# Kernel tuning notes

Hardware: AMD Instinct MI355X
Metric: run time of the kernel (lower is better)

The kernel has to match this reference:

```python
import jax, jax.numpy as jnp
import numpy as np

EMBED = 512
HEADS = 8
HEAD_DIM = EMBED // HEADS
WINDOW = 256
HALF = WINDOW // 2
B, S = 2, 2048


def setup_inputs() -> dict:
    key = jax.random.key(0)
    kv, kk, kq, kw = jax.random.split(key, 4)
    return {
        "values": jax.random.normal(kv, (B, 1, S, EMBED), dtype=jnp.float32),
        "keys": jax.random.normal(kk, (B, 1, S, EMBED), dtype=jnp.float32),
        "query": jax.random.normal(kq, (B, 1, S, EMBED), dtype=jnp.float32),
        "mask": jnp.ones((B, 1, 1, S), dtype=jnp.int32),
        "fc_w": jax.random.normal(kw, (EMBED, EMBED), dtype=jnp.float32) * (1.0 / np.sqrt(EMBED)),
        "fc_b": jnp.zeros((EMBED,), dtype=jnp.float32),
    }


def reference(values, keys, query, mask, fc_w, fc_b):
    b = query.shape[0]
    s = values.shape[2]
    v = values.reshape(b, s, HEADS, HEAD_DIM)
    k = keys.reshape(b, s, HEADS, HEAD_DIM)
    q = query.reshape(b, s, HEADS, HEAD_DIM)
    scale = jnp.float32(EMBED ** 0.5)

    # global token: query 0 attends to all keys
    gq = q[:, 0:1]  # (b,1,h,d)
    ge = jnp.einsum('bqhd,bkhd->bhqk', gq, k)
    ga = jax.nn.softmax(ge / scale, axis=3)
    gout = jnp.einsum('bhqk,bkhd->bqhd', ga, v)  # (b,1,h,d)

    # sliding-window queries (positions 1..s-1, band centered at local index i)
    wq = q[:, 1:]  # (b, s-1, h, d)
    qw = s - 1
    e = jnp.einsum('bqhd,bkhd->bhqk', wq, k)  # (b,h,qw,s)
    i = jnp.arange(qw)[:, None]
    j = jnp.arange(s)[None, :]
    band = (j >= i - HALF) & (j <= i + HALF)  # (qw, s)
    # faithful to original: out-of-band energies are ZERO (not -inf)
    e = jnp.where(band[None, None], e, jnp.float32(0.0))
    e = jnp.where(mask == 0, jnp.float32(-1e20), e)
    a = jax.nn.softmax(e / scale, axis=3)
    lout = jnp.einsum('bhqk,bkhd->bqhd', a, v)  # (b,qw,h,d)

    out = jnp.concatenate([gout, lout], axis=1).reshape(b, s, HEADS * HEAD_DIM)
    return out @ fc_w.T + fc_b
```

## Files before the change

### kernel.cpp

```cpp
#include <hip/hip_runtime.h>
#include <math.h>

#define EMBED 512
#define HEADS 8
#define HDIM 64
#define SLEN 2048
#define BATCH 2
#define HALFW 128
#define NCHUNK 32
#define INV_SCALE 0.044194173824159216f

typedef short bf16x8 __attribute__((ext_vector_type(8)));
typedef short s16x4  __attribute__((ext_vector_type(4)));
typedef float f32x4  __attribute__((ext_vector_type(4)));

#define MFMA16(a, b, c) __builtin_amdgcn_mfma_f32_16x16x32_bf16(a, b, c, 0, 0, 0)

__device__ __forceinline__ short f2bf(float x) {
    union { float f; unsigned u; } v; v.f = x;
    unsigned r = v.u + 0x7FFFu + ((v.u >> 16) & 1u);
    return (short)(r >> 16);
}

__device__ __forceinline__ int lidx(int row, int seg) {
    return (((seg << 6) + (row ^ seg)) << 3);
}

__device__ __forceinline__ void gll16(const short* g, short* l) {
    __builtin_amdgcn_global_load_lds(
        (const __attribute__((address_space(1))) unsigned int*)g,
        (__attribute__((address_space(3))) unsigned int*)l, 16, 0, 0);
}

__device__ __forceinline__ void stage_chunk(const short* s0, const short* s1,
                                            short* d0, short* d1, int t) {
    int off = t * 8;
    int wb  = (t >> 6) * 512;
    gll16(s0 + off,        d0 + wb);
    gll16(s0 + 2048 + off, d0 + 2048 + wb);
    gll16(s1 + off,        d1 + wb);
    gll16(s1 + 2048 + off, d1 + 2048 + wb);
}

__global__ __launch_bounds__(256) void prepass(
    const float* __restrict__ q, const float* __restrict__ k,
    const float* __restrict__ v, const int* __restrict__ mask,
    const float* __restrict__ fcw,
    short* __restrict__ Kbf, short* __restrict__ Vbf, short* __restrict__ Wbf,
    float* __restrict__ gnum_part, float* __restrict__ gden_part,
    float* __restrict__ vsum_part, float* __restrict__ nval_part) {
    int d = blockIdx.x;
    int x = d & 7, i = d >> 3;
    int hb8 = x * 2 + (i >= 36);
    int c   = (i >= 36) ? (i - 36) : i;
    int h = hb8 & 7, b = hb8 >> 3;
    int t = threadIdx.x, w = t >> 6, l = t & 63;

    if (c >= NCHUNK) {
        int nb = b * 4 + (c - NCHUNK);
        size_t base = (size_t)(nb * 8 + h) * 4096;
        #pragma unroll
        for (int p = 0; p < 4; ++p) {
            int idx = p * 256 + t, row = idx >> 4, kg = idx & 15;
            float4 f = *(const float4*)(fcw + (size_t)(nb * 64 + row) * EMBED + h * 64 + kg * 4);
            s16x4 o;
            o[0] = f2bf(f.x); o[1] = f2bf(f.y); o[2] = f2bf(f.z); o[3] = f2bf(f.w);
            *(s16x4*)&Wbf[base + lidx(row, kg >> 1) + (kg & 1) * 4] = o;
        }
        return;
    }

    int j0 = c * 64;
    __shared__ float q0s[HDIM];
    __shared__ float wls[64];
    __shared__ int   m_s[64];
    __shared__ float vbuf[64][68];
    __shared__ float red[4][HDIM];
    __shared__ float redv[4][HDIM];

    if (t < 64) {
        q0s[t] = q[(size_t)b * SLEN * EMBED + h * HDIM + t];
        m_s[t] = mask[b * SLEN + j0 + t];
    }
    __syncthreads();

    size_t fragbase = ((size_t)(b * HEADS + h) * NCHUNK + c) * 4096;

    #pragma unroll
    for (int p = 0; p < 4; ++p) {
        int idx = p * 256 + t, row = idx >> 4, kg = idx & 15;
        float4 f = *(const float4*)(k + ((size_t)b * SLEN + j0 + row) * EMBED + h * HDIM + kg * 4);
        float dot = q0s[kg*4+0]*f.x + q0s[kg*4+1]*f.y + q0s[kg*4+2]*f.z + q0s[kg*4+3]*f.w;
        dot += __shfl_xor(dot, 1, 64);
        dot += __shfl_xor(dot, 2, 64);
        dot += __shfl_xor(dot, 4, 64);
        dot += __shfl_xor(dot, 8, 64);
        if ((t & 15) == 0) wls[row] = __expf(dot * INV_SCALE);
        if (!m_s[row]) f = make_float4(0.f, 0.f, 0.f, 0.f);
        s16x4 o;
        o[0] = f2bf(f.x); o[1] = f2bf(f.y); o[2] = f2bf(f.z); o[3] = f2bf(f.w);
        *(s16x4*)&Kbf[fragbase + lidx(row, kg >> 1) + (kg & 1) * 4] = o;
    }

    #pragma unroll
    for (int p = 0; p < 4; ++p) {
        int idx = p * 256 + t, row = idx >> 4, kg = idx & 15;
        float4 f = *(const float4*)(v + ((size_t)b * SLEN + j0 + row) * EMBED + h * HDIM + kg * 4);
        *(float4*)&vbuf[row][kg * 4] = f;
    }
    __syncthreads();

    float num = 0.f, vs = 0.f;
    #pragma unroll
    for (int jj = 0; jj < 16; ++jj) {
        int jl = w * 16 + jj;
        float vv = vbuf[jl][l];
        num += wls[jl] * vv;
        if (m_s[jl]) vs += vv;
    }
    red[w][l] = num;
    redv[w][l] = vs;

    #pragma unroll
    for (int s = 0; s < 2; ++s) {
        int jseg = w * 2 + s;
        bf16x8 o;
        #pragma unroll
        for (int e = 0; e < 8; ++e) o[e] = f2bf(vbuf[jseg * 8 + e][l]);
        *(bf16x8*)&Vbf[fragbase + lidx(l, jseg)] = o;
    }
    __syncthreads();

    if (w == 0) {
        gnum_part[((size_t)(b * HEADS + h) * NCHUNK + c) * HDIM + l] =
            red[0][l] + red[1][l] + red[2][l] + red[3][l];
        vsum_part[((size_t)b * NCHUNK + c) * EMBED + h * HDIM + l] =
            redv[0][l] + redv[1][l] + redv[2][l] + redv[3][l];
    } else if (w == 1) {
        float s = wls[l];
        #pragma unroll
        for (int off = 32; off > 0; off >>= 1) s += __shfl_xor(s, off, 64);
        if (l == 0) gden_part[(size_t)(b * HEADS + h) * NCHUNK + c] = s;
    } else if (w == 2 && h == 0) {
        float cc = m_s[l] ? 1.f : 0.f;
        #pragma unroll
        for (int off = 32; off > 0; off >>= 1) cc += __shfl_xor(cc, off, 64);
        if (l == 0) nval_part[b * NCHUNK + c] = cc;
    }
}

__global__ __launch_bounds__(256) void windowed_attn_v8(
    const float* __restrict__ q, const float* __restrict__ k,
    const float* __restrict__ v, const int* __restrict__ mask,
    const short* __restrict__ Kbf, const short* __restrict__ Vbf,
    const float* __restrict__ gnum_part, const float* __restrict__ gden_part,
    const float* __restrict__ vsum_part, const float* __restrict__ nval_part,
    short* __restrict__ Abf) {
    int dsp = blockIdx.x;
    int wid = (dsp & 7) * 64 + (dsp >> 3);
    int tile = wid & 31, h = (wid >> 5) & 7, b = wid >> 8;
    int r0 = tile * 64;
    int t = threadIdx.x, w = t >> 6, l = t & 63;
    int lg = l >> 4, lr = l & 15;

    __shared__ __align__(16) short k_s[4][4096];
    __shared__ __align__(16) short v_s[4][4096];
    __shared__ __align__(16) short wT_s[4][16][72];
    __shared__ float rsum[64];
    __shared__ float vred[4][64];
    __shared__ float gred[4][64];
    __shared__ float nv_s, gd_s;

    size_t hb = (size_t)(b * HEADS + h) * NCHUNK;
    int bh = b * HEADS + h;

    int c0 = tile - 2; if (c0 < 0) c0 = 0;
    int c1 = tile + 2; if (c1 > NCHUNK - 1) c1 = NCHUNK - 1;

    stage_chunk(Kbf + (hb + c0) * 4096, Vbf + (hb + c0) * 4096,
                &k_s[0][0], &v_s[0][0], t);

    const float* qrow = q + ((size_t)b * SLEN + r0 + w * 16 + lr) * EMBED + h * HDIM;
    float4 a0 = *(const float4*)(qrow + lg * 8);
    float4 a1 = *(const float4*)(qrow + lg * 8 + 4);
    float4 a2 = *(const float4*)(qrow + 32 + lg * 8);
    float4 a3 = *(const float4*)(qrow + 32 + lg * 8 + 4);
    bf16x8 qb0, qb1;
    qb0[0] = f2bf(a0.x); qb0[1] = f2bf(a0.y); qb0[2] = f2bf(a0.z); qb0[3] = f2bf(a0.w);
    qb0[4] = f2bf(a1.x); qb0[5] = f2bf(a1.y); qb0[6] = f2bf(a1.z); qb0[7] = f2bf(a1.w);
    qb1[0] = f2bf(a2.x); qb1[1] = f2bf(a2.y); qb1[2] = f2bf(a2.z); qb1[3] = f2bf(a2.w);
    qb1[4] = f2bf(a3.x); qb1[5] = f2bf(a3.y); qb1[6] = f2bf(a3.z); qb1[7] = f2bf(a3.w);

    {
        float vp = 0.f;
        #pragma unroll
        for (int cc = 0; cc < 8; ++cc)
            vp += vsum_part[((size_t)b * NCHUNK + w * 8 + cc) * EMBED + h * HDIM + l];
        vred[w][l] = vp;
        if (w == 0) {
            float nvv = (l < NCHUNK) ? nval_part[b * NCHUNK + l] : 0.f;
            #pragma unroll
            for (int off = 32; off > 0; off >>= 1) nvv += __shfl_xor(nvv, off, 64);
            if (l == 0) nv_s = nvv;
        }
        if (tile == 0) {
            float gp = 0.f;
            #pragma unroll
            for (int cc = 0; cc < 8; ++cc)
                gp += gnum_part[((size_t)bh * NCHUNK + w * 8 + cc) * HDIM + l];
            gred[w][l] = gp;
            if (w == 1) {
                float gdd = (l < NCHUNK) ? gden_part[(size_t)bh * NCHUNK + l] : 0.f;
                #pragma unroll
                for (int off = 32; off > 0; off >>= 1) gdd += __shfl_xor(gdd, off, 64);
                if (l == 0) gd_s = gdd;
            }
        }
    }

    stage_chunk(Kbf + (hb + c0 + 1) * 4096, Vbf + (hb + c0 + 1) * 4096,
                &k_s[1][0], &v_s[1][0], t);
    stage_chunk(Kbf + (hb + c0 + 2) * 4096, Vbf + (hb + c0 + 2) * 4096,
                &k_s[2][0], &v_s[2][0], t);

    int center = r0 + w * 16 + lr - 1;
    int lo = center - HALFW, hi = center + HALFW;

    f32x4 pv[4];
    #pragma unroll
    for (int dt = 0; dt < 4; ++dt) pv[dt] = (f32x4){0.f, 0.f, 0.f, 0.f};
    float dacc = 0.f;

    int bi = 0;
    for (int c = c0; c <= c1; ++c) {
        int rem = c1 - c;
        if (rem >= 2)      { asm volatile("s_waitcnt vmcnt(8)" ::: "memory"); }
        else if (rem == 1) { asm volatile("s_waitcnt vmcnt(4)" ::: "memory"); }
        else               { asm volatile("s_waitcnt vmcnt(0)" ::: "memory"); }
        __syncthreads();

        int jc = c * 64;
        #pragma unroll
        for (int jt = 0; jt < 4; ++jt) {
            bf16x8 ka0 = *(const bf16x8*)&k_s[bi][lidx(jt * 16 + lr, lg)];
            bf16x8 ka1 = *(const bf16x8*)&k_s[bi][lidx(jt * 16 + lr, 4 + lg)];
            f32x4 sT = (f32x4){0.f, 0.f, 0.f, 0.f};
            sT = MFMA16(ka0, qb0, sT);
            sT = MFMA16(ka1, qb1, sT);
            int jbase = jc + jt * 16 + lg * 4;
            s16x4 wq;
            #pragma unroll
            for (int r = 0; r < 4; ++r) {
                int j = jbase + r;
                float wgt = (j >= lo && j <= hi) ? (__expf(sT[r] * INV_SCALE) - 1.f) : 0.f;
                dacc += wgt;
                wq[r] = f2bf(wgt);
            }
            *(s16x4*)&wT_s[w][lr][jt * 16 + lg * 4] = wq;
        }

        bf16x8 wa0 = *(const bf16x8*)&wT_s[w][lr][lg * 8];
        bf16x8 wa1 = *(const bf16x8*)&wT_s[w][lr][32 + lg * 8];
        #pragma unroll
        for (int dt = 0; dt < 4; ++dt) {
            bf16x8 va0 = *(const bf16x8*)&v_s[bi][lidx(dt * 16 + lr, lg)];
            bf16x8 va1 = *(const bf16x8*)&v_s[bi][lidx(dt * 16 + lr, 4 + lg)];
            pv[dt] = MFMA16(wa0, va0, pv[dt]);
            pv[dt] = MFMA16(wa1, va1, pv[dt]);
        }

        if (c + 3 <= c1) {
            int bn = (bi + 3) & 3;
            stage_chunk(Kbf + (hb + c + 3) * 4096, Vbf + (hb + c + 3) * 4096,
                        &k_s[bn][0], &v_s[bn][0], t);
        }
        bi = (bi + 1) & 3;
    }

    float wfix = 0.f;
    int jx = r0 - 129;
    if (w == 0 && jx >= 0) {
        float qv = q[((size_t)b * SLEN + r0) * EMBED + h * HDIM + l];
        float kv = k[((size_t)b * SLEN + jx) * EMBED + h * HDIM + l];
        float dd = qv * kv;
        #pragma unroll
        for (int off = 32; off > 0; off >>= 1) dd += __shfl_xor(dd, off, 64);
        if (mask[b * SLEN + jx] != 0) wfix = __expf(dd * INV_SCALE) - 1.f;
        if (lg == 0) {
            #pragma unroll
            for (int dt = 0; dt < 4; ++dt)
                pv[dt][0] += wfix * v[((size_t)b * SLEN + jx) * EMBED + h * HDIM + dt * 16 + lr];
        }
    }

    dacc += __shfl_xor(dacc, 16, 64);
    dacc += __shfl_xor(dacc, 32, 64);
    if (lg == 0) rsum[w * 16 + lr] = dacc + ((w == 0 && lr == 0) ? wfix : 0.f);
    __syncthreads();

    float nv = nv_s;
    float invden[4];
    #pragma unroll
    for (int r = 0; r < 4; ++r)
        invden[r] = 1.f / (nv + rsum[w * 16 + lg * 4 + r]);

    short* Atile = Abf + ((size_t)(b * NCHUNK + tile) * 8 + h) * 4096;
    #pragma unroll
    for (int dt = 0; dt < 4; ++dt) {
        int d = dt * 16 + lr;
        float vs = vred[0][d] + vred[1][d] + vred[2][d] + vred[3][d];
        #pragma unroll
        for (int r = 0; r < 4; ++r) {
            int row_local = w * 16 + lg * 4 + r;
            float o;
            if (tile == 0 && row_local == 0)
                o = (gred[0][d] + gred[1][d] + gred[2][d] + gred[3][d]) / gd_s;
            else
                o = (pv[dt][r] + vs) * invden[r];
            Atile[lidx(row_local, d >> 3) + (d & 7)] = f2bf(o);
        }
    }
}

__global__ __launch_bounds__(256) void fc_gemm_v4(
    const short* __restrict__ Abf, const short* __restrict__ Wbf,
    const float* __restrict__ bias, float* __restrict__ C) {
    int bm = blockIdx.x;
    int nb = blockIdx.y;
    int t = threadIdx.x, w = t >> 6, l = t & 63;
    int lg = l >> 4, lr = l & 15;
    int wr = w >> 1, wc = w & 1;

    __shared__ __align__(16) short a_s[8][4096];
    __shared__ __align__(16) short w_s[2][4096];

    int off = t * 8;
    int wb  = (t >> 6) * 512;

    #pragma unroll
    for (int kt = 0; kt < 8; ++kt) {
        const short* as = Abf + (size_t)(bm * 8 + kt) * 4096;
        gll16(as + off,        &a_s[kt][wb]);
        gll16(as + 2048 + off, &a_s[kt][2048 + wb]);
    }
    {
        const short* ws0 = Wbf + (size_t)(nb * 8 + 0) * 4096;
        gll16(ws0 + off,        &w_s[0][wb]);
        gll16(ws0 + 2048 + off, &w_s[0][2048 + wb]);
        const short* ws1 = Wbf + (size_t)(nb * 8 + 1) * 4096;
        gll16(ws1 + off,        &w_s[1][wb]);
        gll16(ws1 + 2048 + off, &w_s[1][2048 + wb]);
    }

    f32x4 acc[2][2];
    #pragma unroll
    for (int mt = 0; mt < 2; ++mt)
        #pragma unroll
        for (int nt = 0; nt < 2; ++nt) acc[mt][nt] = (f32x4){0.f, 0.f, 0.f, 0.f};

    for (int kt = 0; kt < 8; ++kt) {
        if (kt < 7) { asm volatile("s_waitcnt vmcnt(2)" ::: "memory"); }
        else        { asm volatile("s_waitcnt vmcnt(0)" ::: "memory"); }
        __syncthreads();

        bf16x8 af[2][2], bf_[2][2];
        #pragma unroll
        for (int mt = 0; mt < 2; ++mt) {
            af[mt][0] = *(const bf16x8*)&a_s[kt][lidx(wr * 32 + mt * 16 + lr, lg)];
            af[mt][1] = *(const bf16x8*)&a_s[kt][lidx(wr * 32 + mt * 16 + lr, 4 + lg)];
        }
        int wbuf = kt & 1;
        #pragma unroll
        for (int nt = 0; nt < 2; ++nt) {
            bf_[nt][0] = *(const bf16x8*)&w_s[wbuf][lidx(wc * 32 + nt * 16 + lr, lg)];
            bf_[nt][1] = *(const bf16x8*)&w_s[wbuf][lidx(wc * 32 + nt * 16 + lr, 4 + lg)];
        }
        #pragma unroll
        for (int mt = 0; mt < 2; ++mt)
            #pragma unroll
            for (int nt = 0; nt < 2; ++nt) {
                acc[mt][nt] = MFMA16(af[mt][0], bf_[nt][0], acc[mt][nt]);
                acc[mt][nt] = MFMA16(af[mt][1], bf_[nt][1], acc[mt][nt]);
            }

        __syncthreads();
        if (kt + 2 <= 7) {
            const short* ws = Wbf + (size_t)(nb * 8 + kt + 2) * 4096;
            gll16(ws + off,        &w_s[wbuf][wb]);
            gll16(ws + 2048 + off, &w_s[wbuf][2048 + wb]);
        }
    }

    #pragma unroll
    for (int mt = 0; mt < 2; ++mt)
        #pragma unroll
        for (int nt = 0; nt < 2; ++nt) {
            int n = nb * 64 + wc * 32 + nt * 16 + lr;
            float bb = bias[n];
            #pragma unroll
            for (int reg = 0; reg < 4; ++reg) {
                int m = bm * 64 + wr * 32 + mt * 16 + lg * 4 + reg;
                C[(size_t)m * 512 + n] = acc[mt][nt][reg] + bb;
            }
        }
}

extern "C" void kernel_launch(void* const* d_in, const int* in_sizes, int n_in,
                              void* d_out, int out_size, void* d_ws, size_t ws_size,
                              hipStream_t stream) {
    const float* values = (const float*)d_in[0];
    const float* keys   = (const float*)d_in[1];
    const float* query  = (const float*)d_in[2];
    const int*   maskp  = (const int*)d_in[3];
    const float* fc_w   = (const float*)d_in[4];
    const float* fc_b   = (const float*)d_in[5];
    float* out = (float*)d_out;

    short* Abf = (short*)d_ws;
    short* Wbf = Abf + (size_t)BATCH * SLEN * EMBED;
    short* Kbf = Wbf + (size_t)EMBED * EMBED;
    short* Vbf = Kbf + (size_t)BATCH * HEADS * NCHUNK * 4096;
    float* vsum_part = (float*)(Vbf + (size_t)BATCH * HEADS * NCHUNK * 4096);
    float* gnum_part = vsum_part + (size_t)BATCH * NCHUNK * EMBED;
    float* gden_part = gnum_part + (size_t)BATCH * HEADS * NCHUNK * HDIM;
    float* nval_part = gden_part + (size_t)BATCH * HEADS * NCHUNK;

    prepass<<<dim3(576), 256, 0, stream>>>(
        query, keys, values, maskp, fc_w, Kbf, Vbf, Wbf,
        gnum_part, gden_part, vsum_part, nval_part);
    windowed_attn_v8<<<dim3(512), 256, 0, stream>>>(
        query, keys, values, maskp, Kbf, Vbf,
        gnum_part, gden_part, vsum_part, nval_part, Abf);
    fc_gemm_v4<<<dim3(64, 8), 256, 0, stream>>>(
        Abf, Wbf, fc_b, out);
}
```

Baseline: 31.73 us.

## Split prepass into 32-row half-chunks and issue W tiles before A in GEMM

The prepass now processes 32-key half-chunks per block instead of 64, doubling its grid to 1088 blocks. Partial sums for the global token and vsum double in count, and the attention kernel reduces over 64 partials. The W-conversion blocks are also remapped. In the FC GEMM, the first two W tiles are issued right after the first A tile, with adjusted vmcnt waits, so the first k-steps can start sooner. The cost is more blocks with less work each and more partial-sum traffic.

After: 30.91 us (median of 2 runs). 1.03x faster.

```diff
diff --git a/kernel.cpp b/kernel.cpp
--- a/kernel.cpp
+++ b/kernel.cpp
@@ -40,6 +40,13 @@
     gll16(s0 + 2048 + off, d0 + 2048 + wb);
     gll16(s1 + off,        d1 + wb);
     gll16(s1 + 2048 + off, d1 + 2048 + wb);
+}
+
+__device__ __forceinline__ void stage_tile(const short* s, short* d, int t) {
+    int off = t * 8;
+    int wb  = (t >> 6) * 512;
+    gll16(s + off,        d + wb);
+    gll16(s + 2048 + off, d + 2048 + wb);
 }
 
 __global__ __launch_bounds__(256) void prepass(
@@ -51,18 +58,19 @@
     float* __restrict__ vsum_part, float* __restrict__ nval_part) {
     int d = blockIdx.x;
     int x = d & 7, i = d >> 3;
-    int hb8 = x * 2 + (i >= 36);
-    int c   = (i >= 36) ? (i - 36) : i;
+    int hb8 = x * 2 + (i >= 68);
+    int ii  = (i >= 68) ? (i - 68) : i;
     int h = hb8 & 7, b = hb8 >> 3;
     int t = threadIdx.x, w = t >> 6, l = t & 63;
 
-    if (c >= NCHUNK) {
-        int nb = b * 4 + (c - NCHUNK);
-        size_t base = (size_t)(nb * 8 + h) * 4096;
+    if (ii >= 64) {
+        int widx = hb8 * 4 + (ii - 64);
+        int nb = widx >> 3, kt = widx & 7;
+        size_t base = (size_t)(nb * 8 + kt) * 4096;
         #pragma unroll
         for (int p = 0; p < 4; ++p) {
             int idx = p * 256 + t, row = idx >> 4, kg = idx & 15;
-            float4 f = *(const float4*)(fcw + (size_t)(nb * 64 + row) * EMBED + h * 64 + kg * 4);
+            float4 f = *(const float4*)(fcw + (size_t)(nb * 64 + row) * EMBED + kt * 64 + kg * 4);
             s16x4 o;
             o[0] = f2bf(f.x); o[1] = f2bf(f.y); o[2] = f2bf(f.z); o[3] = f2bf(f.w);
             *(s16x4*)&Wbf[base + lidx(row, kg >> 1) + (kg & 1) * 4] = o;
@@ -70,24 +78,26 @@
         return;
     }
 
-    int j0 = c * 64;
+    int ch  = ii;
+    int c   = ch >> 1;
+    int rof = (ch & 1) * 32;
+    int j0  = ch * 32;
+
     __shared__ float q0s[HDIM];
-    __shared__ float wls[64];
-    __shared__ int   m_s[64];
-    __shared__ float vbuf[64][68];
+    __shared__ float wls[32];
+    __shared__ int   m_s[32];
+    __shared__ float vbuf[32][68];
     __shared__ float red[4][HDIM];
     __shared__ float redv[4][HDIM];
 
-    if (t < 64) {
-        q0s[t] = q[(size_t)b * SLEN * EMBED + h * HDIM + t];
-        m_s[t] = mask[b * SLEN + j0 + t];
-    }
+    if (t < 64) q0s[t] = q[(size_t)b * SLEN * EMBED + h * HDIM + t];
+    else if (t < 96) m_s[t - 64] = mask[b * SLEN + j0 + (t - 64)];
     __syncthreads();
 
     size_t fragbase = ((size_t)(b * HEADS + h) * NCHUNK + c) * 4096;
 
     #pragma unroll
-    for (int p = 0; p < 4; ++p) {
+    for (int p = 0; p < 2; ++p) {
         int idx = p * 256 + t, row = idx >> 4, kg = idx & 15;
         float4 f = *(const float4*)(k + ((size_t)b * SLEN + j0 + row) * EMBED + h * HDIM + kg * 4);
         float dot = q0s[kg*4+0]*f.x + q0s[kg*4+1]*f.y + q0s[kg*4+2]*f.z + q0s[kg*4+3]*f.w;
@@ -99,11 +109,11 @@
         if (!m_s[row]) f = make_float4(0.f, 0.f, 0.f, 0.f);
         s16x4 o;
         o[0] = f2bf(f.x); o[1] = f2bf(f.y); o[2] = f2bf(f.z); o[3] = f2bf(f.w);
-        *(s16x4*)&Kbf[fragbase + lidx(row, kg >> 1) + (kg & 1) * 4] = o;
-    }
-
-    #pragma unroll
-    for (int p = 0; p < 4; ++p) {
+        *(s16x4*)&Kbf[fragbase + lidx(rof + row, kg >> 1) + (kg & 1) * 4] = o;
+    }
+
+    #pragma unroll
+    for (int p = 0; p < 2; ++p) {
         int idx = p * 256 + t, row = idx >> 4, kg = idx & 15;
         float4 f = *(const float4*)(v + ((size_t)b * SLEN + j0 + row) * EMBED + h * HDIM + kg * 4);
         *(float4*)&vbuf[row][kg * 4] = f;
@@ -112,8 +122,8 @@
 
     float num = 0.f, vs = 0.f;
     #pragma unroll
-    for (int jj = 0; jj < 16; ++jj) {
-        int jl = w * 16 + jj;
+    for (int jj = 0; jj < 8; ++jj) {
+        int jl = w * 8 + jj;
         float vv = vbuf[jl][l];
         num += wls[jl] * vv;
         if (m_s[jl]) vs += vv;
@@ -121,35 +131,34 @@
     red[w][l] = num;
     redv[w][l] = vs;
 
-    #pragma unroll
-    for (int s = 0; s < 2; ++s) {
-        int jseg = w * 2 + s;
+    {
+        int jseg = (ch & 1) * 4 + w;
         bf16x8 o;
         #pragma unroll
-        for (int e = 0; e < 8; ++e) o[e] = f2bf(vbuf[jseg * 8 + e][l]);
+        for (int e = 0; e < 8; ++e) o[e] = f2bf(vbuf[w * 8 + e][l]);
         *(bf16x8*)&Vbf[fragbase + lidx(l, jseg)] = o;
     }
     __syncthreads();
 
     if (w == 0) {
-        gnum_part[((size_t)(b * HEADS + h) * NCHUNK + c) * HDIM + l] =
+        gnum_part[((size_t)(b * HEADS + h) * 64 + ch) * HDIM + l] =
             red[0][l] + red[1][l] + red[2][l] + red[3][l];
-        vsum_part[((size_t)b * NCHUNK + c) * EMBED + h * HDIM + l] =
+        vsum_part[((size_t)b * 64 + ch) * EMBED + h * HDIM + l] =
             redv[0][l] + redv[1][l] + redv[2][l] + redv[3][l];
     } else if (w == 1) {
-        float s = wls[l];
+        float s = (l < 32) ? wls[l] : 0.f;
         #pragma unroll
         for (int off = 32; off > 0; off >>= 1) s += __shfl_xor(s, off, 64);
-        if (l == 0) gden_part[(size_t)(b * HEADS + h) * NCHUNK + c] = s;
+        if (l == 0) gden_part[(size_t)(b * HEADS + h) * 64 + ch] = s;
     } else if (w == 2 && h == 0) {
-        float cc = m_s[l] ? 1.f : 0.f;
+        float cc = (l < 32 && m_s[l]) ? 1.f : 0.f;
         #pragma unroll
         for (int off = 32; off > 0; off >>= 1) cc += __shfl_xor(cc, off, 64);
-        if (l == 0) nval_part[b * NCHUNK + c] = cc;
-    }
-}
-
-__global__ __launch_bounds__(256) void windowed_attn_v8(
+        if (l == 0) nval_part[b * 64 + ch] = cc;
+    }
+}
+
+__global__ __launch_bounds__(256) void windowed_attn_v9(
     const float* __restrict__ q, const float* __restrict__ k,
     const float* __restrict__ v, const int* __restrict__ mask,
     const short* __restrict__ Kbf, const short* __restrict__ Vbf,
@@ -194,11 +203,11 @@
     {
         float vp = 0.f;
         #pragma unroll
-        for (int cc = 0; cc < 8; ++cc)
-            vp += vsum_part[((size_t)b * NCHUNK + w * 8 + cc) * EMBED + h * HDIM + l];
+        for (int cc = 0; cc < 16; ++cc)
+            vp += vsum_part[((size_t)b * 64 + w * 16 + cc) * EMBED + h * HDIM + l];
         vred[w][l] = vp;
         if (w == 0) {
-            float nvv = (l < NCHUNK) ? nval_part[b * NCHUNK + l] : 0.f;
+            float nvv = nval_part[b * 64 + l];
             #pragma unroll
             for (int off = 32; off > 0; off >>= 1) nvv += __shfl_xor(nvv, off, 64);
             if (l == 0) nv_s = nvv;
@@ -206,11 +215,11 @@
         if (tile == 0) {
             float gp = 0.f;
             #pragma unroll
-            for (int cc = 0; cc < 8; ++cc)
-                gp += gnum_part[((size_t)bh * NCHUNK + w * 8 + cc) * HDIM + l];
+            for (int cc = 0; cc < 16; ++cc)
+                gp += gnum_part[((size_t)bh * 64 + w * 16 + cc) * HDIM + l];
             gred[w][l] = gp;
             if (w == 1) {
-                float gdd = (l < NCHUNK) ? gden_part[(size_t)bh * NCHUNK + l] : 0.f;
+                float gdd = gden_part[(size_t)bh * 64 + l];
                 #pragma unroll
                 for (int off = 32; off > 0; off >>= 1) gdd += __shfl_xor(gdd, off, 64);
                 if (l == 0) gd_s = gdd;
@@ -322,7 +331,7 @@
     }
 }
 
-__global__ __launch_bounds__(256) void fc_gemm_v4(
+__global__ __launch_bounds__(256) void fc_gemm_v5(
     const short* __restrict__ Abf, const short* __restrict__ Wbf,
     const float* __restrict__ bias, float* __restrict__ C) {
     int bm = blockIdx.x;
@@ -334,33 +343,24 @@
     __shared__ __align__(16) short a_s[8][4096];
     __shared__ __align__(16) short w_s[2][4096];
 
-    int off = t * 8;
-    int wb  = (t >> 6) * 512;
-
-    #pragma unroll
+    stage_tile(Abf + (size_t)(bm * 8 + 0) * 4096, &a_s[0][0], t);
+    stage_tile(Wbf + (size_t)(nb * 8 + 0) * 4096, &w_s[0][0], t);
+    stage_tile(Wbf + (size_t)(nb * 8 + 1) * 4096, &w_s[1][0], t);
+    #pragma unroll
+    for (int kt = 1; kt < 8; ++kt)
+        stage_tile(Abf + (size_t)(bm * 8 + kt) * 4096, &a_s[kt][0], t);
+
+    f32x4 acc[2][2];
+    #pragma unroll
+    for (int mt = 0; mt < 2; ++mt)
+        #pragma unroll
+        for (int nt = 0; nt < 2; ++nt) acc[mt][nt] = (f32x4){0.f, 0.f, 0.f, 0.f};
+
     for (int kt = 0; kt < 8; ++kt) {
-        const short* as = Abf + (size_t)(bm * 8 + kt) * 4096;
-        gll16(as + off,        &a_s[kt][wb]);
-        gll16(as + 2048 + off, &a_s[kt][2048 + wb]);
-    }
-    {
-        const short* ws0 = Wbf + (size_t)(nb * 8 + 0) * 4096;
-        gll16(ws0 + off,        &w_s[0][wb]);
-        gll16(ws0 + 2048 + off, &w_s[0][2048 + wb]);
-        const short* ws1 = Wbf + (size_t)(nb * 8 + 1) * 4096;
-        gll16(ws1 + off,        &w_s[1][wb]);
-        gll16(ws1 + 2048 + off, &w_s[1][2048 + wb]);
-    }
-
-    f32x4 acc[2][2];
-    #pragma unroll
-    for (int mt = 0; mt < 2; ++mt)
-        #pragma unroll
-        for (int nt = 0; nt < 2; ++nt) acc[mt][nt] = (f32x4){0.f, 0.f, 0.f, 0.f};
-
-    for (int kt = 0; kt < 8; ++kt) {
-        if (kt < 7) { asm volatile("s_waitcnt vmcnt(2)" ::: "memory"); }
-        else        { asm volatile("s_waitcnt vmcnt(0)" ::: "memory"); }
+        if (kt == 0)      { asm volatile("s_waitcnt vmcnt(16)" ::: "memory"); }
+        else if (kt == 1) { asm volatile("s_waitcnt vmcnt(14)" ::: "memory"); }
+        else if (kt < 7)  { asm volatile("s_waitcnt vmcnt(2)"  ::: "memory"); }
+        else              { asm volatile("s_waitcnt vmcnt(0)"  ::: "memory"); }
         __syncthreads();
 
         bf16x8 af[2][2], bf_[2][2];
@@ -384,11 +384,8 @@
             }
 
         __syncthreads();
-        if (kt + 2 <= 7) {
-            const short* ws = Wbf + (size_t)(nb * 8 + kt + 2) * 4096;
-            gll16(ws + off,        &w_s[wbuf][wb]);
-            gll16(ws + 2048 + off, &w_s[wbuf][2048 + wb]);
-        }
+        if (kt + 2 <= 7)
+            stage_tile(Wbf + (size_t)(nb * 8 + kt + 2) * 4096, &w_s[wbuf][0], t);
     }
 
     #pragma unroll
@@ -421,16 +418,16 @@
     short* Kbf = Wbf + (size_t)EMBED * EMBED;
     short* Vbf = Kbf + (size_t)BATCH * HEADS * NCHUNK * 4096;
     float* vsum_part = (float*)(Vbf + (size_t)BATCH * HEADS * NCHUNK * 4096);
-    float* gnum_part = vsum_part + (size_t)BATCH * NCHUNK * EMBED;
-    float* gden_part = gnum_part + (size_t)BATCH * HEADS * NCHUNK * HDIM;
-    float* nval_part = gden_part + (size_t)BATCH * HEADS * NCHUNK;
-
-    prepass<<<dim3(576), 256, 0, stream>>>(
+    float* gnum_part = vsum_part + (size_t)BATCH * 64 * EMBED;
+    float* gden_part = gnum_part + (size_t)BATCH * HEADS * 64 * HDIM;
+    float* nval_part = gden_part + (size_t)BATCH * HEADS * 64;
+
+    prepass<<<dim3(1088), 256, 0, stream>>>(
         query, keys, values, maskp, fc_w, Kbf, Vbf, Wbf,
         gnum_part, gden_part, vsum_part, nval_part);
-    windowed_attn_v8<<<dim3(512), 256, 0, stream>>>(
+    windowed_attn_v9<<<dim3(512), 256, 0, stream>>>(
         query, keys, values, maskp, Kbf, Vbf,
         gnum_part, gden_part, vsum_part, nval_part, Abf);
-    fc_gemm_v4<<<dim3(64, 8), 256, 0, stream>>>(
+    fc_gemm_v5<<<dim3(64, 8), 256, 0, stream>>>(
         Abf, Wbf, fc_b, out);
 }
```
